# Kernel optimization log

Measured on AMD Instinct MI355X. Metric: run time of the kernel, lower is better.

Reference implementation:

```python
import jax, jax.numpy as jnp
import numpy as np

R_MAX = 32
S_MAX = 2
C_Z = 128
NTB = 2 * R_MAX + 2 + 1  # num_tok_pos_bins = 67
IN_DIM = 2 * NTB + (2 * S_MAX + 2) + 1  # 141


def _compute_bins(asym_id, entity_id, residue_index, token_index, sym_id, mask):
    # Pairwise [B, N, N] bucket indices, matching the torch module exactly.
    same_chain = asym_id[..., :, None] == asym_id[..., None, :]
    same_entity = entity_id[..., :, None] == entity_id[..., None, :]
    d_res = jnp.where(
        same_chain,
        jnp.clip(residue_index[..., :, None] - residue_index[..., None, :] + R_MAX, 0, 2 * R_MAX),
        2 * R_MAX + 1,
    )
    same_res = residue_index[..., :, None] == residue_index[..., None, :]
    tok_dist = token_index[..., :, None] - token_index[..., None, :] + R_MAX
    d_tok = jnp.where(same_chain & same_res, jnp.clip(tok_dist, 0, 2 * R_MAX), 2 * R_MAX + 1)
    d_chain = jnp.where(
        same_entity,
        jnp.clip(sym_id[..., :, None] - sym_id[..., None, :] + S_MAX, 0, 2 * S_MAX),
        2 * S_MAX + 1,
    )
    # index-removal spoofing: masked pairs go to the last token-position bin
    d_tok = jnp.where(mask, NTB - 1, d_tok)
    d_res = jnp.where(mask, NTB - 1, d_res)
    return d_res, d_tok, same_entity, d_chain


def setup_inputs() -> dict:
    key = jax.random.key(0)
    ks = jax.random.split(key, 7)
    B, N = 1, 768
    asym_id = jax.random.randint(ks[0], (B, N), 0, 4, dtype=jnp.int32)
    entity_id = jax.random.randint(ks[1], (B, N), 0, 3, dtype=jnp.int32)
    residue_index = jnp.sort(jax.random.randint(ks[2], (B, N), 0, 200, dtype=jnp.int32), axis=-1)
    token_index = jnp.sort(jax.random.randint(ks[3], (B, N), 0, 300, dtype=jnp.int32), axis=-1)
    sym_id = jax.random.randint(ks[4], (B, N), 0, 4, dtype=jnp.int32)
    unindexing_pair_mask = jax.random.randint(ks[5], (B, N, N), 0, 2) > 0
    W = jax.random.normal(ks[6], (IN_DIM, C_Z), dtype=jnp.float32) * 0.02
    return {
        "asym_id": asym_id,
        "entity_id": entity_id,
        "residue_index": residue_index,
        "token_index": token_index,
        "sym_id": sym_id,
        "unindexing_pair_mask": unindexing_pair_mask,
        "W": W,
    }


def reference(asym_id, entity_id, residue_index, token_index, sym_id, unindexing_pair_mask, W):
    d_res, d_tok, same_entity, d_chain = _compute_bins(
        asym_id, entity_id, residue_index, token_index, sym_id, unindexing_pair_mask
    )
    # linear(one_hot concat) == gather-sum of weight row blocks (same math, fused):
    # concat layout: [relpos (NTB) | reltoken (NTB) | same_entity (1) | relchain (2*S_MAX+2)]
    W_res = W[:NTB]                      # [67, c_z]
    W_tok = W[NTB:2 * NTB]               # [67, c_z]
    w_ent = W[2 * NTB]                   # [c_z]
    W_chain = W[2 * NTB + 1:]            # [6, c_z]
    out = (
        W_res[d_res]
        + W_tok[d_tok]
        + same_entity.astype(W.dtype)[..., None] * w_ent
        + W_chain[d_chain]
    )  # [B, N, N, c_z]
    return out
```

## Files before the change

kernel.cpp:

```cpp
#include <hip/hip_runtime.h>

#define R_MAX 32
#define S_MAX 2
#define C_Z   128
#define NTB   (2 * R_MAX + 2 + 1)
#define IN_DIM (2 * NTB + (2 * S_MAX + 2) + 1)
#define JT   256

typedef float vf4 __attribute__((ext_vector_type(4)));

__device__ __forceinline__ int clampi(int x, int lo, int hi) {
    return min(max(x, lo), hi);
}

__global__ __launch_bounds__(256) void relpos_kernel(
    const int* __restrict__ asym_id,
    const int* __restrict__ entity_id,
    const int* __restrict__ residue_index,
    const int* __restrict__ token_index,
    const int* __restrict__ sym_id,
    const int* __restrict__ mask,
    const float* __restrict__ W,
    float* __restrict__ out,
    int N)
{
    __shared__ int codeT[JT];

    const int tid = threadIdx.x;
    const int row = blockIdx.y;
    const int jb  = blockIdx.x * JT;
    const int b   = row / N;

    const int ai = asym_id[row];
    const int ei = entity_id[row];
    const int ri = residue_index[row];
    const int ti = token_index[row];
    const int si = sym_id[row];

    {
        int j = jb + tid;
        int code = 0;
        if (j < N) {
            int jrow = b * N + j;
            int aj = asym_id[jrow];
            int ej = entity_id[jrow];
            int rj = residue_index[jrow];
            int tj = token_index[jrow];
            int sj = sym_id[jrow];

            bool same_chain  = (ai == aj);
            bool same_entity = (ei == ej);
            bool same_res    = (ri == rj);

            int d_res   = same_chain ? clampi(ri - rj + R_MAX, 0, 2 * R_MAX) : (2 * R_MAX + 1);
            int d_tok   = (same_chain && same_res) ? clampi(ti - tj + R_MAX, 0, 2 * R_MAX)
                                                   : (2 * R_MAX + 1);
            int d_chain = same_entity ? clampi(si - sj + S_MAX, 0, 2 * S_MAX) : (2 * S_MAX + 1);

            if (mask[(long long)row * N + j] != 0) { d_res = NTB - 1; d_tok = NTB - 1; }

            code = d_res | (d_tok << 7) | (d_chain << 14) | (same_entity ? (1 << 17) : 0);
        }
        codeT[(tid & 7) * 32 + (tid >> 3)] = code;
    }
    __syncthreads();

    const int chunk = tid & 31;
    const int psub  = tid >> 5;
    const vf4* __restrict__ W4 = (const vf4*)W + chunk;

    const vf4 e = W4[(2 * NTB) * 32];

    vf4* __restrict__ outp = (vf4*)out + ((long long)row * N + jb) * 32 + chunk;
    const int jmax = min(JT, N - jb);

    int4 creg[8];
    {
        const int4* cp = (const int4*)&codeT[psub * 32];
        #pragma unroll
        for (int k = 0; k < 8; ++k) creg[k] = cp[k];
    }

#define PROC(codev, itv)                                                      \
    {                                                                         \
        int code    = (codev);                                                \
        int pair    = (itv) * 8 + psub;                                       \
        int d_res   = code & 127;                                             \
        int d_tok   = (code >> 7) & 127;                                      \
        int d_chain = (code >> 14) & 7;                                       \
        float se    = (float)((code >> 17) & 1);                              \
        vf4 r  = W4[d_res * 32];                                              \
        vf4 t  = W4[(NTB + d_tok) * 32];                                      \
        vf4 cc = W4[(2 * NTB + 1 + d_chain) * 32];                            \
        vf4 o  = r + t + se * e + cc;                                         \
        __builtin_nontemporal_store(o, &outp[pair * 32]);                     \
    }

    if (jmax == JT) {
        #pragma unroll
        for (int k = 0; k < 8; ++k) {
            int4 c = creg[k];
            PROC(c.x, 4 * k + 0)
            PROC(c.y, 4 * k + 1)
            PROC(c.z, 4 * k + 2)
            PROC(c.w, 4 * k + 3)
        }
    } else {
        #pragma unroll
        for (int k = 0; k < 8; ++k) {
            int4 c = creg[k];
            if (4 * k * 8 + psub < jmax)       PROC(c.x, 4 * k + 0)
            if ((4 * k + 1) * 8 + psub < jmax) PROC(c.y, 4 * k + 1)
            if ((4 * k + 2) * 8 + psub < jmax) PROC(c.z, 4 * k + 2)
            if ((4 * k + 3) * 8 + psub < jmax) PROC(c.w, 4 * k + 3)
        }
    }
#undef PROC
}

extern "C" void kernel_launch(void* const* d_in, const int* in_sizes, int n_in,
                              void* d_out, int out_size, void* d_ws, size_t ws_size,
                              hipStream_t stream) {
    const int*   asym_id       = (const int*)d_in[0];
    const int*   entity_id     = (const int*)d_in[1];
    const int*   residue_index = (const int*)d_in[2];
    const int*   token_index   = (const int*)d_in[3];
    const int*   sym_id        = (const int*)d_in[4];
    const int*   mask          = (const int*)d_in[5];
    const float* W             = (const float*)d_in[6];
    float*       out           = (float*)d_out;

    long long BN      = in_sizes[0];
    long long mask_sz = in_sizes[5];
    int N = (int)(mask_sz / BN);

    dim3 grid((unsigned)((N + JT - 1) / JT), (unsigned)BN);
    dim3 block(256);

    relpos_kernel<<<grid, block, 0, stream>>>(
        asym_id, entity_id, residue_index, token_index, sym_id,
        mask, W, out, N);
}
```

Before: 319.8 us.

## Precombine weight rows into a case table in LDS to cut per-pair gathers

The three bin gathers plus the entity term are replaced by one lookup in a 48-row table of combined weight rows, indexed by mask, chain, residue, entity and chain-bin case. At most one extra global gather is added for the free residue or token offset. A small pre-kernel builds the table in workspace when workspace is large enough; otherwise each block builds it from W. Each block also now handles two rows, and the output stores are no longer nontemporal. This trades 24KB of LDS per block, which may lower occupancy, for fewer gathers and less arithmetic per output vector.

Result: no change. 320.0 us (+0.1%).

```diff
diff --git a/kernel.cpp b/kernel.cpp
--- a/kernel.cpp
+++ b/kernel.cpp
@@ -3,9 +3,11 @@
 #define R_MAX 32
 #define S_MAX 2
 #define C_Z   128
-#define NTB   (2 * R_MAX + 2 + 1)
-#define IN_DIM (2 * NTB + (2 * S_MAX + 2) + 1)
+#define NTB   67
+#define IN_DIM 141
 #define JT   256
+#define IR   2
+#define TROWS 48
 
 typedef float vf4 __attribute__((ext_vector_type(4)));
 
@@ -13,131 +15,147 @@
     return min(max(x, lo), hi);
 }
 
+__device__ __forceinline__ vf4 table_entry(const vf4* __restrict__ W4, int r, int c) {
+    int g  = r % 12, cls = r / 12;
+    int se = g / 6,  dc  = g % 6;
+    vf4 v;
+    if (cls == 0)      v = W4[66*32 + c] + W4[(NTB + 66)*32 + c];
+    else if (cls == 1) v = W4[65*32 + c] + W4[(NTB + 65)*32 + c];
+    else if (cls == 2) v = W4[(NTB + 65)*32 + c];
+    else               v = W4[32*32 + c];
+    v = v + W4[(2*NTB + 1 + dc)*32 + c];
+    if (se) v = v + W4[(2*NTB)*32 + c];
+    return v;
+}
+
+__global__ __launch_bounds__(256) void table_kernel(const float* __restrict__ W,
+                                                    float* __restrict__ ws) {
+    int idx = blockIdx.x * 256 + threadIdx.x;
+    ((vf4*)ws)[idx] = table_entry((const vf4*)W, idx >> 5, idx & 31);
+}
+
 __global__ __launch_bounds__(256) void relpos_kernel(
-    const int* __restrict__ asym_id,
-    const int* __restrict__ entity_id,
-    const int* __restrict__ residue_index,
-    const int* __restrict__ token_index,
-    const int* __restrict__ sym_id,
-    const int* __restrict__ mask,
-    const float* __restrict__ W,
-    float* __restrict__ out,
-    int N)
+    const int* __restrict__ asym, const int* __restrict__ ent,
+    const int* __restrict__ res,  const int* __restrict__ tok,
+    const int* __restrict__ sym,  const int* __restrict__ mask,
+    const float* __restrict__ W,  const float* __restrict__ ws,
+    float* __restrict__ out, int N, int BN, int use_ws)
 {
-    __shared__ int codeT[JT];
+    __shared__ vf4 table_s[TROWS * 32];
+    __shared__ __align__(16) int codeT[IR * JT];
 
-    const int tid = threadIdx.x;
-    const int row = blockIdx.y;
-    const int jb  = blockIdx.x * JT;
-    const int b   = row / N;
+    const int tid  = threadIdx.x;
+    const int jb   = blockIdx.x * JT;
+    const int row0 = blockIdx.y * IR;
+    const vf4* __restrict__ W4 = (const vf4*)W;
 
-    const int ai = asym_id[row];
-    const int ei = entity_id[row];
-    const int ri = residue_index[row];
-    const int ti = token_index[row];
-    const int si = sym_id[row];
+    if (use_ws) {
+        const vf4* __restrict__ ws4 = (const vf4*)ws;
+        #pragma unroll
+        for (int k = 0; k < 6; ++k) { int idx = tid + k*256; table_s[idx] = ws4[idx]; }
+    } else {
+        #pragma unroll
+        for (int k = 0; k < 6; ++k) { int idx = tid + k*256; table_s[idx] = table_entry(W4, idx >> 5, idx & 31); }
+    }
 
     {
         int j = jb + tid;
-        int code = 0;
-        if (j < N) {
-            int jrow = b * N + j;
-            int aj = asym_id[jrow];
-            int ej = entity_id[jrow];
-            int rj = residue_index[jrow];
-            int tj = token_index[jrow];
-            int sj = sym_id[jrow];
-
-            bool same_chain  = (ai == aj);
-            bool same_entity = (ei == ej);
-            bool same_res    = (ri == rj);
-
-            int d_res   = same_chain ? clampi(ri - rj + R_MAX, 0, 2 * R_MAX) : (2 * R_MAX + 1);
-            int d_tok   = (same_chain && same_res) ? clampi(ti - tj + R_MAX, 0, 2 * R_MAX)
-                                                   : (2 * R_MAX + 1);
-            int d_chain = same_entity ? clampi(si - sj + S_MAX, 0, 2 * S_MAX) : (2 * S_MAX + 1);
-
-            if (mask[(long long)row * N + j] != 0) { d_res = NTB - 1; d_tok = NTB - 1; }
-
-            code = d_res | (d_tok << 7) | (d_chain << 14) | (same_entity ? (1 << 17) : 0);
+        bool jok = (j < N);
+        for (int ir = 0; ir < IR; ++ir) {
+            int row = row0 + ir;
+            int code = 0;
+            if (jok && row < BN) {
+                int b    = row / N;
+                int jrow = b * N + j;
+                int aj = asym[jrow], ej = ent[jrow], rj = res[jrow], tj = tok[jrow], sj = sym[jrow];
+                int ai = asym[row],  ei = ent[row],  ri = res[row],  ti = tok[row],  si = sym[row];
+                bool sc = (ai == aj), sent = (ei == ej), sr = (ri == rj);
+                int dc = sent ? clampi(si - sj + S_MAX, 0, 2*S_MAX) : (2*S_MAX + 1);
+                int g  = (sent ? 6 : 0) + dc;
+                bool m = mask[(long long)row * N + j] != 0;
+                int lrow, grow;
+                if (m)        { lrow = g;        grow = 0; }
+                else if (!sc) { lrow = 12 + g;   grow = 0; }
+                else if (!sr) { lrow = 24 + g;   grow = 1 + clampi(ri - rj + R_MAX, 0, 2*R_MAX); }
+                else          { lrow = 36 + g;   grow = 1 + NTB + clampi(ti - tj + R_MAX, 0, 2*R_MAX); }
+                code = lrow | (grow << 6);
+            }
+            codeT[ir * JT + (tid & 7) * 32 + (tid >> 3)] = code;
         }
-        codeT[(tid & 7) * 32 + (tid >> 3)] = code;
     }
     __syncthreads();
 
     const int chunk = tid & 31;
     const int psub  = tid >> 5;
-    const vf4* __restrict__ W4 = (const vf4*)W + chunk;
+    const int jmax  = min(JT, N - jb);
 
-    const vf4 e = W4[(2 * NTB) * 32];
+    for (int ir = 0; ir < IR; ++ir) {
+        int row = row0 + ir;
+        if (row >= BN) break;
+        vf4* __restrict__ outp = (vf4*)out + ((long long)row * N + jb) * 32 + chunk;
 
-    vf4* __restrict__ outp = (vf4*)out + ((long long)row * N + jb) * 32 + chunk;
-    const int jmax = min(JT, N - jb);
-
-    int4 creg[8];
-    {
-        const int4* cp = (const int4*)&codeT[psub * 32];
+        int4 creg[8];
+        const int4* cp = (const int4*)&codeT[ir * JT + psub * 32];
         #pragma unroll
         for (int k = 0; k < 8; ++k) creg[k] = cp[k];
-    }
 
 #define PROC(codev, itv)                                                      \
-    {                                                                         \
-        int code    = (codev);                                                \
-        int pair    = (itv) * 8 + psub;                                       \
-        int d_res   = code & 127;                                             \
-        int d_tok   = (code >> 7) & 127;                                      \
-        int d_chain = (code >> 14) & 7;                                       \
-        float se    = (float)((code >> 17) & 1);                              \
-        vf4 r  = W4[d_res * 32];                                              \
-        vf4 t  = W4[(NTB + d_tok) * 32];                                      \
-        vf4 cc = W4[(2 * NTB + 1 + d_chain) * 32];                            \
-        vf4 o  = r + t + se * e + cc;                                         \
-        __builtin_nontemporal_store(o, &outp[pair * 32]);                     \
+        {                                                                     \
+            int code = (codev);                                               \
+            int pair = (itv) * 8 + psub;                                      \
+            int lrow = code & 63;                                             \
+            int grow = code >> 6;                                             \
+            vf4 acc  = table_s[lrow * 32 + chunk];                            \
+            if (grow) acc += W4[(grow - 1) * 32 + chunk];                     \
+            outp[pair * 32] = acc;                                            \
+        }
+
+        if (jmax == JT) {
+            #pragma unroll
+            for (int k = 0; k < 8; ++k) {
+                int4 c = creg[k];
+                PROC(c.x, 4*k + 0)
+                PROC(c.y, 4*k + 1)
+                PROC(c.z, 4*k + 2)
+                PROC(c.w, 4*k + 3)
+            }
+        } else {
+            #pragma unroll
+            for (int k = 0; k < 8; ++k) {
+                int4 c = creg[k];
+                if (4*k*8 + psub < jmax)       PROC(c.x, 4*k + 0)
+                if ((4*k + 1)*8 + psub < jmax) PROC(c.y, 4*k + 1)
+                if ((4*k + 2)*8 + psub < jmax) PROC(c.z, 4*k + 2)
+                if ((4*k + 3)*8 + psub < jmax) PROC(c.w, 4*k + 3)
+            }
+        }
+#undef PROC
     }
-
-    if (jmax == JT) {
-        #pragma unroll
-        for (int k = 0; k < 8; ++k) {
-            int4 c = creg[k];
-            PROC(c.x, 4 * k + 0)
-            PROC(c.y, 4 * k + 1)
-            PROC(c.z, 4 * k + 2)
-            PROC(c.w, 4 * k + 3)
-        }
-    } else {
-        #pragma unroll
-        for (int k = 0; k < 8; ++k) {
-            int4 c = creg[k];
-            if (4 * k * 8 + psub < jmax)       PROC(c.x, 4 * k + 0)
-            if ((4 * k + 1) * 8 + psub < jmax) PROC(c.y, 4 * k + 1)
-            if ((4 * k + 2) * 8 + psub < jmax) PROC(c.z, 4 * k + 2)
-            if ((4 * k + 3) * 8 + psub < jmax) PROC(c.w, 4 * k + 3)
-        }
-    }
-#undef PROC
 }
 
 extern "C" void kernel_launch(void* const* d_in, const int* in_sizes, int n_in,
                               void* d_out, int out_size, void* d_ws, size_t ws_size,
                               hipStream_t stream) {
-    const int*   asym_id       = (const int*)d_in[0];
-    const int*   entity_id     = (const int*)d_in[1];
-    const int*   residue_index = (const int*)d_in[2];
-    const int*   token_index   = (const int*)d_in[3];
-    const int*   sym_id        = (const int*)d_in[4];
-    const int*   mask          = (const int*)d_in[5];
-    const float* W             = (const float*)d_in[6];
-    float*       out           = (float*)d_out;
+    const int*   asym = (const int*)d_in[0];
+    const int*   ent  = (const int*)d_in[1];
+    const int*   res  = (const int*)d_in[2];
+    const int*   tok  = (const int*)d_in[3];
+    const int*   sym  = (const int*)d_in[4];
+    const int*   mask = (const int*)d_in[5];
+    const float* W    = (const float*)d_in[6];
+    float*       out  = (float*)d_out;
 
     long long BN      = in_sizes[0];
     long long mask_sz = in_sizes[5];
     int N = (int)(mask_sz / BN);
 
-    dim3 grid((unsigned)((N + JT - 1) / JT), (unsigned)BN);
-    dim3 block(256);
+    int use_ws = (ws_size >= (size_t)(TROWS * 32 * sizeof(vf4))) ? 1 : 0;
+    if (use_ws) {
+        table_kernel<<<6, 256, 0, stream>>>(W, (float*)d_ws);
+    }
 
-    relpos_kernel<<<grid, block, 0, stream>>>(
-        asym_id, entity_id, residue_index, token_index, sym_id,
-        mask, W, out, N);
+    dim3 grid((unsigned)((N + JT - 1) / JT), (unsigned)((BN + IR - 1) / IR));
+    relpos_kernel<<<grid, 256, 0, stream>>>(
+        asym, ent, res, tok, sym, mask, W, (const float*)d_ws, out,
+        N, (int)BN, use_ws);
 }
```
